# Kernel optimization log

Measured on AMD Instinct MI355X. Metric: run time of the kernel, lower is better.

## Reference

```python
import jax, jax.numpy as jnp
import numpy as np

IM_FE_RATIO = 16.0


def setup_inputs() -> dict:
    key = jax.random.key(0)
    k1, k2 = jax.random.split(key)
    B, C, H, W, N = 4, 128, 256, 256, 4096
    feature = jax.random.normal(k1, (B, C, H, W), dtype=jnp.float32)
    # keypoints in image-pixel coords, in range [0, (W-1)*im_fe_ratio]
    keypoints = jax.random.uniform(k2, (B, N, 2), dtype=jnp.float32,
                                   minval=0.0, maxval=(W - 1) * IM_FE_RATIO)
    return {"feature": feature, "keypoints": keypoints}


def _interpolate(feature, keypoints):
    B, C, H, W = feature.shape
    kp = keypoints / IM_FE_RATIO  # B x N x 2 in feature-map coords (x, y)
    max_xy = jnp.array([W - 1, H - 1], dtype=kp.dtype)
    lo = jnp.maximum(jnp.floor(kp), 0.0)   # B x N x 2
    hi = jnp.minimum(jnp.ceil(kp), max_xy)  # B x N x 2
    up = kp - lo                            # fractional part (weight for upper corner)
    lw = 1.0 - up                           # weight for lower corner

    # corner order matches torch code: (x0,y0), (x1,y0), (x0,y1), (x1,y1)
    ix = jnp.stack([lo[..., 0], hi[..., 0], lo[..., 0], hi[..., 0]], axis=-1).astype(jnp.int32)  # B x N x 4
    iy = jnp.stack([lo[..., 1], lo[..., 1], hi[..., 1], hi[..., 1]], axis=-1).astype(jnp.int32)  # B x N x 4
    wx = jnp.stack([lw[..., 0], up[..., 0], lw[..., 0], up[..., 0]], axis=-1)
    wy = jnp.stack([lw[..., 1], lw[..., 1], up[..., 1], up[..., 1]], axis=-1)
    coeff = wx * wy                          # B x N x 4

    idx = (iy * W + ix)                      # B x N x 4 flat spatial indices
    feat_flat = feature.reshape(B, C, H * W)

    # gather per batch: (C, HW)[:, (N,4)] -> C x N x 4
    gathered = jax.vmap(lambda f, i: f[:, i])(feat_flat, idx)  # B x C x N x 4
    uf = jnp.einsum('bcnk,bnk->bcn', gathered, coeff)          # B x C x N

    # mask off keypoints that are (0, 0): mean over the 2 coords of (kp > 1e-10)
    mask = (kp > 1e-10).astype(uf.dtype).mean(axis=2)          # B x N
    return uf * mask[:, None, :]


def reference(feature, keypoints):
    return _interpolate(feature, keypoints)
```

## Files before the change

### kernel.cpp

```cpp
#include <hip/hip_runtime.h>

#define BB 4
#define CC 128
#define HH 256
#define WW 256
#define NKP 4096
#define INV_RATIO (1.0f / 16.0f)
#define CPT 4
#define NXCD 8

typedef float fpair __attribute__((ext_vector_type(2)));

__global__ __launch_bounds__(256) void interp_kernel(
    const float* __restrict__ feature,
    const float* __restrict__ keypoints,
    float* __restrict__ out)
{
    int bid   = blockIdx.x;
    int xcd   = bid & (NXCD - 1);
    int slot  = bid >> 3;
    int gloc  = slot >> 4;
    int j     = slot & 15;
    int g     = gloc * NXCD + xcd;
    int b     = g >> 5;
    int c0    = (g & 31) * CPT;
    int n     = j * 256 + threadIdx.x;

    const float* kp = keypoints + ((size_t)(b * NKP + n)) * 2;
    float kx = kp[0] * INV_RATIO;
    float ky = kp[1] * INV_RATIO;

    float fx = fmaxf(floorf(kx), 0.0f);
    float fy = fmaxf(floorf(ky), 0.0f);
    int x0 = (int)fx, y0 = (int)fy;

    float ux = kx - fx, uy = ky - fy;
    float lx = 1.0f - ux, ly = 1.0f - uy;

    bool selx = (x0 >= WW - 1);
    bool sely = (y0 >= HH - 1);
    int xp = selx ? (WW - 2) : x0;
    int yp = sely ? (HH - 2) : y0;
    float wlx = selx ? 0.0f : lx, wux = selx ? 1.0f : ux;
    float wly = sely ? 0.0f : ly, wuy = sely ? 1.0f : uy;

    float mask = 0.5f * ((kx > 1e-10f ? 1.0f : 0.0f) + (ky > 1e-10f ? 1.0f : 0.0f));
    float w00 = wlx * wly * mask, w01 = wux * wly * mask;
    float w10 = wlx * wuy * mask, w11 = wux * wuy * mask;

    int i0 = yp * WW + xp;
    int i1 = i0 + WW;

    const float* f = feature + ((size_t)(b * CC + c0)) * (HH * WW);

    fpair r0[CPT], r1[CPT];
    #pragma unroll
    for (int k = 0; k < CPT; ++k) {
        const float* fc = f + (size_t)k * (HH * WW);
        __builtin_memcpy(&r0[k], fc + i0, sizeof(fpair));
        __builtin_memcpy(&r1[k], fc + i1, sizeof(fpair));
    }

    float* o = out + ((size_t)(b * CC + c0)) * NKP + n;
    #pragma unroll
    for (int k = 0; k < CPT; ++k) {
        float val = w00 * r0[k].x + w01 * r0[k].y
                  + w10 * r1[k].x + w11 * r1[k].y;
        __builtin_nontemporal_store(val, o + (size_t)k * NKP);
    }
}

extern "C" void kernel_launch(void* const* d_in, const int* in_sizes, int n_in,
                              void* d_out, int out_size, void* d_ws, size_t ws_size,
                              hipStream_t stream) {
    const float* feature   = (const float*)d_in[0];
    const float* keypoints = (const float*)d_in[1];
    float* out = (float*)d_out;

    const int grid = BB * (CC / CPT) * (NKP / 256);
    interp_kernel<<<grid, 256, 0, stream>>>(feature, keypoints, out);
}
```

Before: 30.39 us.

## Stream feature slabs into cache via LDS-dump prefetch before bilinear gathers

The kernel now runs a fixed grid of 1024 blocks. Each block loops over four channel-group tiles and issues global_load_lds bulk loads that sweep the contiguous feature slab into a throwaway LDS buffer. The goal is to warm the cache with streaming accesses, so the scattered 8-byte corner gathers that follow hit in cache instead of going to DRAM randomly. Work is also regrouped so each thread handles 2 channels for one of 128 keypoints, instead of 4 channels for one of 256. The cost is extra load instructions and LDS traffic, and nothing orders the prefetch ahead of the gathers, so the two may race.

Result: slower. 36.42 us (+19.9%).

```diff
diff --git a/kernel.cpp b/kernel.cpp
--- a/kernel.cpp
+++ b/kernel.cpp
@@ -8,65 +8,87 @@
 #define INV_RATIO (1.0f / 16.0f)
 #define CPT 4
 #define NXCD 8
+#define JBLK 32
+#define CHUNK 128
+#define TILES 4
 
 typedef float fpair __attribute__((ext_vector_type(2)));
+typedef const __attribute__((address_space(1))) void gvoid;
+typedef __attribute__((address_space(3))) void svoid;
 
-__global__ __launch_bounds__(256) void interp_kernel(
+__global__ __launch_bounds__(256) void interp_pf_kernel(
     const float* __restrict__ feature,
     const float* __restrict__ keypoints,
     float* __restrict__ out)
 {
-    int bid   = blockIdx.x;
-    int xcd   = bid & (NXCD - 1);
-    int slot  = bid >> 3;
-    int gloc  = slot >> 4;
-    int j     = slot & 15;
-    int g     = gloc * NXCD + xcd;
-    int b     = g >> 5;
-    int c0    = (g & 31) * CPT;
-    int n     = j * 256 + threadIdx.x;
+    __shared__ float dump[4][256];
 
-    const float* kp = keypoints + ((size_t)(b * NKP + n)) * 2;
-    float kx = kp[0] * INV_RATIO;
-    float ky = kp[1] * INV_RATIO;
+    int bid  = blockIdx.x;
+    int xcd  = bid & (NXCD - 1);
+    int s    = bid >> 3;
+    int c    = s >> 5;
+    int j    = s & 31;
+    int tid  = threadIdx.x;
+    int w    = tid >> 6, lane = tid & 63;
 
-    float fx = fmaxf(floorf(kx), 0.0f);
-    float fy = fmaxf(floorf(ky), 0.0f);
-    int x0 = (int)fx, y0 = (int)fy;
+    int kpi  = tid & (CHUNK - 1);
+    int ch2  = (tid >> 7) & 1;
 
-    float ux = kx - fx, uy = ky - fy;
-    float lx = 1.0f - ux, ly = 1.0f - uy;
+    for (int t = 0; t < TILES; ++t) {
+        int gloc = c * TILES + t;
+        int g    = gloc * NXCD + xcd;
+        int b    = g >> 5;
+        int c0   = (g & 31) * CPT;
 
-    bool selx = (x0 >= WW - 1);
-    bool sely = (y0 >= HH - 1);
-    int xp = selx ? (WW - 2) : x0;
-    int yp = sely ? (HH - 2) : y0;
-    float wlx = selx ? 0.0f : lx, wux = selx ? 1.0f : ux;
-    float wly = sely ? 0.0f : ly, wuy = sely ? 1.0f : uy;
+        const float* fg = feature + (size_t)(b * CC + c0) * (HH * WW);
 
-    float mask = 0.5f * ((kx > 1e-10f ? 1.0f : 0.0f) + (ky > 1e-10f ? 1.0f : 0.0f));
-    float w00 = wlx * wly * mask, w01 = wux * wly * mask;
-    float w10 = wlx * wuy * mask, w11 = wux * wuy * mask;
+        const char* pbase = (const char*)fg
+                          + ((size_t)j << 15) + ((size_t)w << 13) + ((size_t)lane << 4);
+        svoid* ldst = (svoid*)&dump[w][0];
+        #pragma unroll
+        for (int r = 0; r < 8; ++r) {
+            __builtin_amdgcn_global_load_lds((gvoid*)(pbase + (r << 10)), ldst, 16, 0, 0);
+        }
 
-    int i0 = yp * WW + xp;
-    int i1 = i0 + WW;
+        int n = j * CHUNK + kpi;
+        const float* kp = keypoints + ((size_t)(b * NKP + n)) * 2;
+        float kx = kp[0] * INV_RATIO;
+        float ky = kp[1] * INV_RATIO;
 
-    const float* f = feature + ((size_t)(b * CC + c0)) * (HH * WW);
+        float fx = fmaxf(floorf(kx), 0.0f);
+        float fy = fmaxf(floorf(ky), 0.0f);
+        int x0 = (int)fx, y0 = (int)fy;
 
-    fpair r0[CPT], r1[CPT];
-    #pragma unroll
-    for (int k = 0; k < CPT; ++k) {
-        const float* fc = f + (size_t)k * (HH * WW);
-        __builtin_memcpy(&r0[k], fc + i0, sizeof(fpair));
-        __builtin_memcpy(&r1[k], fc + i1, sizeof(fpair));
-    }
+        float ux = kx - fx, uy = ky - fy;
+        float lx = 1.0f - ux, ly = 1.0f - uy;
 
-    float* o = out + ((size_t)(b * CC + c0)) * NKP + n;
-    #pragma unroll
-    for (int k = 0; k < CPT; ++k) {
-        float val = w00 * r0[k].x + w01 * r0[k].y
-                  + w10 * r1[k].x + w11 * r1[k].y;
-        __builtin_nontemporal_store(val, o + (size_t)k * NKP);
+        bool selx = (x0 >= WW - 1);
+        bool sely = (y0 >= HH - 1);
+        int xp = selx ? (WW - 2) : x0;
+        int yp = sely ? (HH - 2) : y0;
+        float wlx = selx ? 0.0f : lx, wux = selx ? 1.0f : ux;
+        float wly = sely ? 0.0f : ly, wuy = sely ? 1.0f : uy;
+
+        float mask = 0.5f * ((kx > 1e-10f ? 1.0f : 0.0f) + (ky > 1e-10f ? 1.0f : 0.0f));
+        float w00 = wlx * wly * mask, w01 = wux * wly * mask;
+        float w10 = wlx * wuy * mask, w11 = wux * wuy * mask;
+
+        int i0 = yp * WW + xp;
+        int i1 = i0 + WW;
+
+        const float* fc = fg + (size_t)(2 * ch2) * (HH * WW);
+        fpair a0, a1, b0, b1;
+        __builtin_memcpy(&a0, fc + i0, sizeof(fpair));
+        __builtin_memcpy(&a1, fc + i1, sizeof(fpair));
+        __builtin_memcpy(&b0, fc + (HH * WW) + i0, sizeof(fpair));
+        __builtin_memcpy(&b1, fc + (HH * WW) + i1, sizeof(fpair));
+
+        float v0 = w00 * a0.x + w01 * a0.y + w10 * a1.x + w11 * a1.y;
+        float v1 = w00 * b0.x + w01 * b0.y + w10 * b1.x + w11 * b1.y;
+
+        float* o = out + (size_t)(b * CC + c0 + 2 * ch2) * NKP + n;
+        __builtin_nontemporal_store(v0, o);
+        __builtin_nontemporal_store(v1, o + NKP);
     }
 }
 
@@ -77,6 +99,5 @@
     const float* keypoints = (const float*)d_in[1];
     float* out = (float*)d_out;
 
-    const int grid = BB * (CC / CPT) * (NKP / 256);
-    interp_kernel<<<grid, 256, 0, stream>>>(feature, keypoints, out);
+    interp_pf_kernel<<<1024, 256, 0, stream>>>(feature, keypoints, out);
 }
```
